# Performance work log

Hardware: AMD Instinct MI355X
Metric: run time of the kernel (lower is better)

Reference implementation:

```python
import jax, jax.numpy as jnp
import numpy as np

G = 32          # grid_size
H = 12          # num_heads
D = 768         # embed_dim
HD = D // H     # head_dim = 64
FF = 3072       # ff_dim
B, T = 2, 2048
SPAN = 2 * G - 1        # 63
SPAN_C = 4 * G + 1      # 129
EPS = 1e-5


def setup_inputs() -> dict:
    key = jax.random.key(0)
    ks = jax.random.split(key, 16)
    s = 0.02
    is_sep = jax.random.uniform(ks[6], (T,)) < 0.05
    demo_id = jax.random.randint(ks[5], (T,), 0, 8)
    demo_id = jnp.where(is_sep, -1, demo_id)
    return {
        'x': jax.random.normal(ks[0], (B, T, D), jnp.float32),
        'row': jax.random.randint(ks[1], (T,), 0, G),
        'col': jax.random.randint(ks[2], (T,), 0, G),
        'demo_row': jax.random.randint(ks[3], (T,), 0, G),
        'demo_col': jax.random.randint(ks[4], (T,), 0, 2 * G),
        'demo_id': demo_id,
        'is_sep': is_sep,
        'ln1_w': jnp.ones((D,), jnp.float32),
        'ln1_b': jnp.zeros((D,), jnp.float32),
        'ln2_w': jnp.ones((D,), jnp.float32),
        'ln2_b': jnp.zeros((D,), jnp.float32),
        'qkv_w': jax.random.normal(ks[7], (D, 3 * D), jnp.float32) * s,
        'qkv_b': jnp.zeros((3 * D,), jnp.float32),
        'proj_w': jax.random.normal(ks[8], (D, D), jnp.float32) * s,
        'proj_b': jnp.zeros((D,), jnp.float32),
        'ff1_w': jax.random.normal(ks[9], (D, FF), jnp.float32) * s,
        'ff1_b': jnp.zeros((FF,), jnp.float32),
        'ff2_w': jax.random.normal(ks[10], (FF, D), jnp.float32) * s,
        'ff2_b': jnp.zeros((D,), jnp.float32),
        'rel_emb': jax.random.normal(ks[11], (SPAN * SPAN, H), jnp.float32) * s,
        'demo_emb': jax.random.normal(ks[12], (SPAN_C * SPAN, H), jnp.float32) * s,
    }


def _ln(x, w, b):
    m = jnp.mean(x, -1, keepdims=True)
    v = jnp.mean((x - m) ** 2, -1, keepdims=True)
    return (x - m) / jnp.sqrt(v + EPS) * w + b


def _rel_bias(rel_emb, row, col, is_sep):
    g1 = G - 1
    dr = jnp.clip(row[:, None] - row[None, :], -g1, g1) + g1
    dc = jnp.clip(col[:, None] - col[None, :], -g1, g1) + g1
    bias = rel_emb[dr * SPAN + dc]              # (T, T, H)
    valid = ~is_sep
    vp = (valid[:, None] & valid[None, :]).astype(jnp.float32)
    return jnp.transpose(bias, (2, 0, 1)) * vp[None]  # (H, T, T)


def _demo_bias(demo_emb, drow, dcol, did, is_sep):
    g1 = G - 1
    dr = jnp.clip(drow[:, None] - drow[None, :], -g1, g1) + g1
    dc = jnp.clip(dcol[:, None] - dcol[None, :], -2 * G, 2 * G) + 2 * G
    bias = demo_emb[dr * SPAN_C + dc]           # (T, T, H)
    valid = ~is_sep
    same = (did[:, None] == did[None, :]) & (did[:, None] >= 0) & (did[None, :] >= 0)
    vp = (valid[:, None] & valid[None, :] & same).astype(jnp.float32)
    return jnp.transpose(bias, (2, 0, 1)) * vp[None]


def reference(x, row, col, demo_row, demo_col, demo_id, is_sep,
              ln1_w, ln1_b, ln2_w, ln2_b, qkv_w, qkv_b, proj_w, proj_b,
              ff1_w, ff1_b, ff2_w, ff2_b, rel_emb, demo_emb):
    b, t, d = x.shape
    h1 = _ln(x, ln1_w, ln1_b)
    qkv = h1 @ qkv_w + qkv_b                        # (B, T, 3D)
    q, k, v = jnp.split(qkv, 3, axis=-1)
    q = q.reshape(b, t, H, HD).transpose(0, 2, 1, 3)  # (B, H, T, HD)
    k = k.reshape(b, t, H, HD).transpose(0, 2, 1, 3)
    v = v.reshape(b, t, H, HD).transpose(0, 2, 1, 3)
    scale = float(HD) ** -0.5
    logits = jnp.einsum('bhqd,bhkd->bhqk', q, k) * scale
    bias = _rel_bias(rel_emb, row, col, is_sep) + _demo_bias(demo_emb, demo_row, demo_col, demo_id, is_sep)
    attn = jax.nn.softmax(logits + bias[None], axis=-1)
    out = jnp.einsum('bhqk,bhkd->bhqd', attn, v)
    out = out.transpose(0, 2, 1, 3).reshape(b, t, D)
    out = out @ proj_w + proj_b
    x = x + out
    h2 = _ln(x, ln2_w, ln2_b)
    ff = jax.nn.gelu(h2 @ ff1_w + ff1_b, approximate=False) @ ff2_w + ff2_b
    return x + ff
```

## Files before the change

kernel.cpp:

```cpp
#include <hip/hip_runtime.h>
#include <hip/hip_bf16.h>
#include <hip/hip_fp16.h>
#include <math.h>

#define G_ 32
#define H_ 12
#define D_ 768
#define HD_ 64
#define FF_ 3072
#define B_ 2
#define T_ 2048
#define SPAN_ 63
#define SPANC_ 129
#define EPSF 1e-5f

typedef short bf16x8 __attribute__((ext_vector_type(8)));
typedef short short4v __attribute__((ext_vector_type(4)));
typedef float f32x4 __attribute__((ext_vector_type(4)));

__device__ __forceinline__ short f2bf(float f) {
    unsigned u = __builtin_bit_cast(unsigned, f);
    u = u + 0x7FFFu + ((u >> 16) & 1u);
    return (short)(u >> 16);
}

__device__ __forceinline__ unsigned char f2e5m2(float f) {
    unsigned short u = __half_as_ushort(__float2half(f));
    u = (unsigned short)(u + 0x7F + ((u >> 8) & 1));
    return (unsigned char)(u >> 8);
}
__device__ __forceinline__ float e5m2f(unsigned u) {
    return __half2float(__ushort_as_half((unsigned short)(u << 8)));
}

__device__ __forceinline__ void gl_lds16(const void* g, void* l) {
    __builtin_amdgcn_global_load_lds(
        (const __attribute__((address_space(1))) unsigned int*)g,
        (__attribute__((address_space(3))) unsigned int*)l, 16, 0, 0);
}

__global__ __launch_bounds__(256) void ln_bf16_kernel(const float* __restrict__ x,
                                                      const float* __restrict__ w,
                                                      const float* __restrict__ b,
                                                      short* __restrict__ out) {
    int wv = threadIdx.x >> 6;
    int lane = threadIdx.x & 63;
    int rowi = blockIdx.x * 4 + wv;
    const float* xr = x + (size_t)rowi * D_;
    float vals[12];
    float s = 0.f;
#pragma unroll
    for (int i = 0; i < 12; ++i) { vals[i] = xr[lane + i * 64]; s += vals[i]; }
#pragma unroll
    for (int off = 32; off > 0; off >>= 1) s += __shfl_xor(s, off, 64);
    float mean = s * (1.0f / D_);
    float vs = 0.f;
#pragma unroll
    for (int i = 0; i < 12; ++i) { float d = vals[i] - mean; vs += d * d; }
#pragma unroll
    for (int off = 32; off > 0; off >>= 1) vs += __shfl_xor(vs, off, 64);
    float rstd = rsqrtf(vs * (1.0f / D_) + EPSF);
    short* outr = out + (size_t)rowi * D_;
#pragma unroll
    for (int i = 0; i < 12; ++i) {
        int c = lane + i * 64;
        outr[c] = f2bf((vals[i] - mean) * rstd * w[c] + b[c]);
    }
}

__global__ __launch_bounds__(256) void tcast_all(const float* __restrict__ qkv_w,
                                                 const float* __restrict__ proj_w,
                                                 const float* __restrict__ ff1_w,
                                                 const float* __restrict__ ff2_w,
                                                 short* __restrict__ qkvt,
                                                 short* __restrict__ projt,
                                                 short* __restrict__ ff1t,
                                                 short* __restrict__ ff2t) {
    __shared__ float t[32][33];
    int bid = blockIdx.x;
    const float* W;
    short* Wt;
    int K, N, bx, lo;
    if (bid < 1728)      { W = qkv_w;  Wt = qkvt;  K = D_;  N = 3 * D_; bx = 72; lo = 0; }
    else if (bid < 2304) { W = proj_w; Wt = projt; K = D_;  N = D_;     bx = 24; lo = 1728; }
    else if (bid < 4608) { W = ff1_w;  Wt = ff1t;  K = D_;  N = FF_;    bx = 96; lo = 2304; }
    else                 { W = ff2_w;  Wt = ff2t;  K = FF_; N = D_;     bx = 24; lo = 4608; }
    int rblk = bid - lo;
    int n0 = (rblk % bx) * 32, k0 = (rblk / bx) * 32;
    int tid = threadIdx.x;
    int r = tid >> 3, c4 = (tid & 7) * 4;
    float4 v = *(const float4*)(W + (size_t)(k0 + r) * N + n0 + c4);
    t[r][c4 + 0] = v.x; t[r][c4 + 1] = v.y; t[r][c4 + 2] = v.z; t[r][c4 + 3] = v.w;
    __syncthreads();
    short4v o;
    o[0] = f2bf(t[c4 + 0][r]); o[1] = f2bf(t[c4 + 1][r]);
    o[2] = f2bf(t[c4 + 2][r]); o[3] = f2bf(t[c4 + 3][r]);
    *(short4v*)(Wt + (size_t)(n0 + r) * K + k0 + c4) = o;
}

__global__ __launch_bounds__(256) void bias_build(
    const int* __restrict__ rowp, const int* __restrict__ colp,
    const int* __restrict__ drowp, const int* __restrict__ dcolp,
    const int* __restrict__ didp,
    const float* __restrict__ rel_emb, const float* __restrict__ demo_emb,
    unsigned char* __restrict__ biasT) {
    __shared__ unsigned char patch[12][16][80];
    int k0 = blockIdx.x * 64, q0 = blockIdx.y * 16;
    int tid = threadIdx.x;
    int qi = tid >> 4, kq = (tid & 15) * 4;
    int q = q0 + qi;
    int idq = didp[q];
    int rq = rowp[q], cq = colp[q], drq = drowp[q], dcq = dcolp[q];
    float bvs[4][12];
#pragma unroll
    for (int j = 0; j < 4; ++j) {
        int k = k0 + kq + j;
        int idk = didp[k];
        float4 v0 = {0.f, 0.f, 0.f, 0.f}, v1 = v0, v2 = v0;
        if (idq >= 0 && idk >= 0) {
            int dr = min(max(rq - rowp[k], -(G_ - 1)), G_ - 1) + (G_ - 1);
            int dc = min(max(cq - colp[k], -(G_ - 1)), G_ - 1) + (G_ - 1);
            const float* rp = rel_emb + (size_t)(dr * SPAN_ + dc) * 12;
            v0 = *(const float4*)rp;
            v1 = *(const float4*)(rp + 4);
            v2 = *(const float4*)(rp + 8);
            if (idq == idk) {
                int ddr = min(max(drq - drowp[k], -(G_ - 1)), G_ - 1) + (G_ - 1);
                int ddc = min(max(dcq - dcolp[k], -2 * G_), 2 * G_) + 2 * G_;
                const float* dp = demo_emb + (size_t)(ddr * SPANC_ + ddc) * 12;
                float4 w0 = *(const float4*)dp;
                float4 w1 = *(const float4*)(dp + 4);
                float4 w2 = *(const float4*)(dp + 8);
                v0.x += w0.x; v0.y += w0.y; v0.z += w0.z; v0.w += w0.w;
                v1.x += w1.x; v1.y += w1.y; v1.z += w1.z; v1.w += w1.w;
                v2.x += w2.x; v2.y += w2.y; v2.z += w2.z; v2.w += w2.w;
            }
        }
        bvs[j][0] = v0.x; bvs[j][1] = v0.y; bvs[j][2] = v0.z; bvs[j][3] = v0.w;
        bvs[j][4] = v1.x; bvs[j][5] = v1.y; bvs[j][6] = v1.z; bvs[j][7] = v1.w;
        bvs[j][8] = v2.x; bvs[j][9] = v2.y; bvs[j][10] = v2.z; bvs[j][11] = v2.w;
    }
#pragma unroll
    for (int h = 0; h < 12; ++h) {
        uchar4 pk;
        pk.x = f2e5m2(bvs[0][h]); pk.y = f2e5m2(bvs[1][h]);
        pk.z = f2e5m2(bvs[2][h]); pk.w = f2e5m2(bvs[3][h]);
        *(uchar4*)&patch[h][qi][kq] = pk;
    }
    __syncthreads();
    for (int c = tid; c < 768; c += 256) {
        int rowid = c >> 2, off = (c & 3) * 16;
        int h = rowid >> 4, q2 = rowid & 15;
        *(uint4*)(biasT + (size_t)h * T_ * T_ + (size_t)(q0 + q2) * T_ + k0 + off) =
            *(const uint4*)&patch[h][q2][off];
    }
}

enum { EPI_NONE = 0, EPI_RES = 1, EPI_GELU = 2 };

template <int EPI, int BF16OUT, int BM>
__global__ __launch_bounds__(256, 2) void gemm_bf16(const short* __restrict__ A,
                                                    const short* __restrict__ Bt,
                                                    const float* __restrict__ bias,
                                                    const float* __restrict__ res,
                                                    void* __restrict__ Cv,
                                                    int M, int N, int K) {
    __shared__ short As[BM * 64];
    __shared__ short Bs[128 * 64];
    constexpr int WM = BM / 2;
    constexpr int MF = WM / 16;
    int tid = threadIdx.x;
    int l = tid & 63;
    int w = tid >> 6;
    int wm = w >> 1, wn = w & 1;
    int row0 = blockIdx.y * BM, col0 = blockIdx.x * 128;
    int g = l >> 4, c16 = l & 15;
    f32x4 zero = {0.f, 0.f, 0.f, 0.f};
    f32x4 acc[MF][4];
#pragma unroll
    for (int m = 0; m < MF; ++m)
#pragma unroll
        for (int n = 0; n < 4; ++n) acc[m][n] = zero;

    int srowA = w * (BM / 4) + (l >> 3);
    int srowB = w * 32 + (l >> 3);
    int sseg0 = (l & 7);

    for (int k0 = 0; k0 < K; k0 += 64) {
#pragma unroll
        for (int inst = 0; inst < BM / 32; ++inst) {
            int arow = srowA + inst * 8;
            int seg = sseg0 ^ (arow & 7);
            gl_lds16(A + (size_t)(row0 + arow) * K + k0 + seg * 8,
                     &As[(w * (BM / 4) + inst * 8) * 64]);
        }
#pragma unroll
        for (int inst = 0; inst < 4; ++inst) {
            int brow = srowB + inst * 8;
            int seg = sseg0 ^ (brow & 7);
            gl_lds16(Bt + (size_t)(col0 + brow) * K + k0 + seg * 8,
                     &Bs[(w * 32 + inst * 8) * 64]);
        }
        __syncthreads();
#pragma unroll
        for (int dk = 0; dk < 2; ++dk) {
            bf16x8 af[MF], bfr[4];
#pragma unroll
            for (int m = 0; m < MF; ++m) {
                int r = wm * WM + m * 16 + c16;
                af[m] = *(const bf16x8*)&As[r * 64 + (((dk * 4 + g) ^ (r & 7)) << 3)];
            }
#pragma unroll
            for (int n = 0; n < 4; ++n) {
                int r = wn * 64 + n * 16 + c16;
                bfr[n] = *(const bf16x8*)&Bs[r * 64 + (((dk * 4 + g) ^ (r & 7)) << 3)];
            }
#pragma unroll
            for (int m = 0; m < MF; ++m)
#pragma unroll
                for (int n = 0; n < 4; ++n)
                    acc[m][n] = __builtin_amdgcn_mfma_f32_16x16x32_bf16(af[m], bfr[n], acc[m][n], 0, 0, 0);
        }
        __syncthreads();
    }

#pragma unroll
    for (int m = 0; m < MF; ++m)
#pragma unroll
        for (int n = 0; n < 4; ++n) {
            int rrow = row0 + wm * WM + m * 16 + g * 4;
            int ccol = col0 + wn * 64 + n * 16 + c16;
            float bv = bias[ccol];
#pragma unroll
            for (int i = 0; i < 4; ++i) {
                float v = acc[m][n][i] + bv;
                if (EPI == EPI_GELU) v = 0.5f * v * (1.f + erff(v * 0.70710678118f));
                if (EPI == EPI_RES) v += res[(size_t)(rrow + i) * N + ccol];
                if (BF16OUT)
                    ((short*)Cv)[(size_t)(rrow + i) * N + ccol] = f2bf(v);
                else
                    ((float*)Cv)[(size_t)(rrow + i) * N + ccol] = v;
            }
        }
}

__global__ __launch_bounds__(256, 3) void attn_mfma(
    const short* __restrict__ qkv,
    const unsigned char* __restrict__ biasT,
    short* __restrict__ attn_o) {
    __shared__ short Ks[2][64 * 64];
    __shared__ short Vt[2][64 * 72];
    __shared__ short Pb[4][16 * 72];

    int tid = threadIdx.x, w = tid >> 6, l = tid & 63;
    int g = l >> 4, c16 = l & 15;
    int bid = blockIdx.x;
    int nb = (bid & 7) * 96 + (bid >> 3);
    int qt = nb & 31, bh = nb >> 5;
    int h = bh % H_, b = bh / H_;
    int q0 = qt * 64;
    const int QS = 3 * D_;
    const short* kvbase = qkv + (size_t)b * T_ * QS;

    bf16x8 qf[2];
    {
        int qrow = q0 + w * 16 + c16;
        const short* qp = kvbase + (size_t)qrow * QS + h * HD_;
        qf[0] = *(const bf16x8*)(qp + g * 8);
        qf[1] = *(const bf16x8*)(qp + 32 + g * 8);
    }
    const unsigned char* bptr[4];
#pragma unroll
    for (int i = 0; i < 4; ++i)
        bptr[i] = biasT + (size_t)h * T_ * T_ + (size_t)(q0 + w * 16 + g * 4 + i) * T_;

    int krow = tid >> 3, kseg = tid & 7;
    int kx = (kseg ^ (krow & 7)) << 3;
    const short* kgp = kvbase + D_ + h * HD_ + kseg * 8;
    int vk0 = (tid & 31) * 2, vd0 = (tid >> 5) * 8;
    int vbase = ((((vk0 >> 3) ^ (vd0 >> 3)) & 7) << 3) + (vk0 & 7);
    const short* vgp = kvbase + 2 * D_ + h * HD_ + vd0;

    f32x4 zero = {0.f, 0.f, 0.f, 0.f};
    f32x4 oacc[4];
#pragma unroll
    for (int nf = 0; nf < 4; ++nf) oacc[nf] = zero;
    float lsum[4] = {0.f, 0.f, 0.f, 0.f};

    bf16x8 kr0, kr1, vr0, vr1;
    kr0 = *(const bf16x8*)(kgp + (size_t)krow * QS);
    kr1 = *(const bf16x8*)(kgp + (size_t)(krow + 32) * QS);
    vr0 = *(const bf16x8*)(vgp + (size_t)vk0 * QS);
    vr1 = *(const bf16x8*)(vgp + (size_t)(vk0 + 1) * QS);
    *(bf16x8*)&Ks[0][krow * 64 + kx] = kr0;
    *(bf16x8*)&Ks[0][(krow + 32) * 64 + kx] = kr1;
#pragma unroll
    for (int j = 0; j < 8; ++j) {
        unsigned pr = (unsigned)(ushort)vr0[j] | ((unsigned)(ushort)vr1[j] << 16);
        *(unsigned*)&Vt[0][(vd0 + j) * 72 + vbase] = pr;
    }
    {
        const short* kg1 = kgp + (size_t)64 * QS;
        const short* vg1 = vgp + (size_t)64 * QS;
        kr0 = *(const bf16x8*)(kg1 + (size_t)krow * QS);
        kr1 = *(const bf16x8*)(kg1 + (size_t)(krow + 32) * QS);
        vr0 = *(const bf16x8*)(vg1 + (size_t)vk0 * QS);
        vr1 = *(const bf16x8*)(vg1 + (size_t)(vk0 + 1) * QS);
    }

    for (int t = 0; t < 32; ++t) {
        __syncthreads();
        const short* KsC = Ks[t & 1];
        const short* VtC = Vt[t & 1];
        short* KsN = Ks[(t + 1) & 1];
        short* VtN = Vt[(t + 1) & 1];
        *(bf16x8*)&KsN[krow * 64 + kx] = kr0;
        *(bf16x8*)&KsN[(krow + 32) * 64 + kx] = kr1;
#pragma unroll
        for (int j = 0; j < 8; ++j) {
            unsigned pr = (unsigned)(ushort)vr0[j] | ((unsigned)(ushort)vr1[j] << 16);
            *(unsigned*)&VtN[(vd0 + j) * 72 + vbase] = pr;
        }
        {
            int kb2 = ((t + 2) & 31) * 64;
            const short* kg2 = kgp + (size_t)kb2 * QS;
            const short* vg2 = vgp + (size_t)kb2 * QS;
            kr0 = *(const bf16x8*)(kg2 + (size_t)krow * QS);
            kr1 = *(const bf16x8*)(kg2 + (size_t)(krow + 32) * QS);
            vr0 = *(const bf16x8*)(vg2 + (size_t)vk0 * QS);
            vr1 = *(const bf16x8*)(vg2 + (size_t)(vk0 + 1) * QS);
        }
        int kb = t * 64;
        float bv[16];
#pragma unroll
        for (int nf = 0; nf < 4; ++nf)
#pragma unroll
            for (int i = 0; i < 4; ++i)
                bv[nf * 4 + i] = e5m2f(bptr[i][kb + nf * 16 + c16]);
        f32x4 sac[4];
#pragma unroll
        for (int nf = 0; nf < 4; ++nf) sac[nf] = zero;
#pragma unroll
        for (int dk = 0; dk < 2; ++dk) {
#pragma unroll
            for (int nf = 0; nf < 4; ++nf) {
                int r = nf * 16 + c16;
                bf16x8 kf = *(const bf16x8*)&KsC[r * 64 + (((dk * 4 + g) ^ (r & 7)) << 3)];
                sac[nf] = __builtin_amdgcn_mfma_f32_16x16x32_bf16(qf[dk], kf, sac[nf], 0, 0, 0);
            }
        }
#pragma unroll
        for (int nf = 0; nf < 4; ++nf)
#pragma unroll
            for (int i = 0; i < 4; ++i) {
                float e = __expf(fmaf(sac[nf][i], 0.125f, bv[nf * 4 + i]));
                sac[nf][i] = e;
                lsum[i] += e;
            }
        short* pbw = &Pb[w][0];
#pragma unroll
        for (int nf = 0; nf < 4; ++nf) {
            int chunkbase = nf * 2 + (c16 >> 3);
            int kpos = c16 & 7;
#pragma unroll
            for (int i = 0; i < 4; ++i)
                pbw[(g * 4 + i) * 72 + (((chunkbase ^ g) & 7) << 3) + kpos] = f2bf(sac[nf][i]);
        }
#pragma unroll
        for (int dk = 0; dk < 2; ++dk) {
            bf16x8 pa = *(const bf16x8*)&pbw[c16 * 72 + (((dk * 4 + g) ^ (c16 >> 2)) & 7) * 8];
#pragma unroll
            for (int nf = 0; nf < 4; ++nf) {
                int d = nf * 16 + c16;
                bf16x8 vb = *(const bf16x8*)&VtC[d * 72 + (((dk * 4 + g) ^ (d >> 3)) & 7) * 8];
                oacc[nf] = __builtin_amdgcn_mfma_f32_16x16x32_bf16(pa, vb, oacc[nf], 0, 0, 0);
            }
        }
    }

#pragma unroll
    for (int i = 0; i < 4; ++i) {
#pragma unroll
        for (int off = 1; off < 16; off <<= 1) lsum[i] += __shfl_xor(lsum[i], off, 64);
    }

#pragma unroll
    for (int nf = 0; nf < 4; ++nf)
#pragma unroll
        for (int i = 0; i < 4; ++i) {
            float o = oacc[nf][i] / lsum[i];
            int qq = q0 + w * 16 + g * 4 + i;
            attn_o[(size_t)(b * T_ + qq) * D_ + h * HD_ + nf * 16 + c16] = f2bf(o);
        }
}

extern "C" void kernel_launch(void* const* d_in, const int* in_sizes, int n_in,
                              void* d_out, int out_size, void* d_ws, size_t ws_size,
                              hipStream_t stream) {
    const float* x = (const float*)d_in[0];
    const int* rowp = (const int*)d_in[1];
    const int* colp = (const int*)d_in[2];
    const int* drowp = (const int*)d_in[3];
    const int* dcolp = (const int*)d_in[4];
    const int* didp = (const int*)d_in[5];
    const float* ln1_w = (const float*)d_in[7];
    const float* ln1_b = (const float*)d_in[8];
    const float* ln2_w = (const float*)d_in[9];
    const float* ln2_b = (const float*)d_in[10];
    const float* qkv_w = (const float*)d_in[11];
    const float* qkv_b = (const float*)d_in[12];
    const float* proj_w = (const float*)d_in[13];
    const float* proj_b = (const float*)d_in[14];
    const float* ff1_w = (const float*)d_in[15];
    const float* ff1_b = (const float*)d_in[16];
    const float* ff2_w = (const float*)d_in[17];
    const float* ff2_b = (const float*)d_in[18];
    const float* rel_emb = (const float*)d_in[19];
    const float* demo_emb = (const float*)d_in[20];
    float* out = (float*)d_out;

    const int M = B_ * T_;
    char* p = (char*)d_ws;
    short* h1 = (short*)p;     p += (size_t)M * D_ * 2;
    short* qkvb = (short*)p;   p += (size_t)M * 3 * D_ * 2;
    short* attn_o = (short*)p; p += (size_t)M * D_ * 2;
    short* qkvt = (short*)p;   p += (size_t)(3 * D_) * D_ * 2;
    short* projt = (short*)p;  p += (size_t)D_ * D_ * 2;
    short* ff1t = (short*)p;   p += (size_t)FF_ * D_ * 2;
    short* ff2t = (short*)p;   p += (size_t)D_ * FF_ * 2;
    float* x2 = (float*)p;
    short* h2 = (short*)(p + (size_t)M * D_ * 4);
    short* ffact = (short*)(p + (size_t)M * D_ * 4 + (size_t)M * D_ * 2);
    unsigned char* biasT = (unsigned char*)p;

    bias_build<<<dim3(T_ / 64, T_ / 16), 256, 0, stream>>>(
        rowp, colp, drowp, dcolp, didp, rel_emb, demo_emb, biasT);
    tcast_all<<<dim3(6912), 256, 0, stream>>>(qkv_w, proj_w, ff1_w, ff2_w,
                                              qkvt, projt, ff1t, ff2t);

    ln_bf16_kernel<<<dim3(M / 4), 256, 0, stream>>>(x, ln1_w, ln1_b, h1);

    gemm_bf16<EPI_NONE, 1, 128><<<dim3(3 * D_ / 128, M / 128), 256, 0, stream>>>(
        h1, qkvt, qkv_b, nullptr, qkvb, M, 3 * D_, D_);

    attn_mfma<<<dim3(B_ * H_ * (T_ / 64)), 256, 0, stream>>>(qkvb, biasT, attn_o);

    gemm_bf16<EPI_RES, 0, 64><<<dim3(D_ / 128, M / 64), 256, 0, stream>>>(
        attn_o, projt, proj_b, x, x2, M, D_, D_);

    ln_bf16_kernel<<<dim3(M / 4), 256, 0, stream>>>(x2, ln2_w, ln2_b, h2);

    gemm_bf16<EPI_GELU, 1, 128><<<dim3(FF_ / 128, M / 128), 256, 0, stream>>>(
        h2, ff1t, ff1_b, nullptr, ffact, M, FF_, D_);

    gemm_bf16<EPI_RES, 0, 64><<<dim3(D_ / 128, M / 64), 256, 0, stream>>>(
        ffact, ff2t, ff2_b, x2, out, M, D_, FF_);
}
```

Baseline: 238.7 us.

## Pre-transpose V into global buffer and load V fragments directly in attention

Adds a separate kernel that writes V transposed per (batch, head) into a new workspace buffer. The attention kernel then loads V MFMA operands straight from global memory each tile, dropping the LDS V staging, the in-register transpose and the V double buffer. Launch bounds rise from 3 to 4 waves per SIMD to use the freed LDS. The costs are an extra kernel launch, an extra round trip of V through memory, and uncoalesced strided per-lane global loads inside the loop with less latency hiding.

```diff
diff --git a/kernel.cpp b/kernel.cpp
--- a/kernel.cpp
+++ b/kernel.cpp
@@ -98,6 +98,23 @@
     *(short4v*)(Wt + (size_t)(n0 + r) * K + k0 + c4) = o;
 }
 
+__global__ __launch_bounds__(256) void vtrans_kernel(const short* __restrict__ qkvb,
+                                                     short* __restrict__ vt) {
+    __shared__ short t[32][36];
+    int bh = blockIdx.y;
+    int h = bh % H_, b = bh / H_;
+    int kt = blockIdx.x & 63, dt = blockIdx.x >> 6;
+    int k0 = kt * 32, d0 = dt * 32;
+    int tid = threadIdx.x;
+    int r = tid >> 3, c4 = (tid & 7) * 4;
+    *(short4v*)&t[r][c4] = *(const short4v*)(
+        qkvb + (size_t)(b * T_ + k0 + r) * (3 * D_) + 2 * D_ + h * HD_ + d0 + c4);
+    __syncthreads();
+    short4v o;
+    o[0] = t[c4 + 0][r]; o[1] = t[c4 + 1][r]; o[2] = t[c4 + 2][r]; o[3] = t[c4 + 3][r];
+    *(short4v*)(vt + (size_t)((b * H_ + h) * HD_ + d0 + r) * T_ + k0 + c4) = o;
+}
+
 __global__ __launch_bounds__(256) void bias_build(
     const int* __restrict__ rowp, const int* __restrict__ colp,
     const int* __restrict__ drowp, const int* __restrict__ dcolp,
@@ -244,12 +261,12 @@
         }
 }
 
-__global__ __launch_bounds__(256, 3) void attn_mfma(
+__global__ __launch_bounds__(256, 4) void attn_mfma(
     const short* __restrict__ qkv,
+    const short* __restrict__ vt,
     const unsigned char* __restrict__ biasT,
     short* __restrict__ attn_o) {
     __shared__ short Ks[2][64 * 64];
-    __shared__ short Vt[2][64 * 72];
     __shared__ short Pb[4][16 * 72];
 
     int tid = threadIdx.x, w = tid >> 6, l = tid & 63;
@@ -274,12 +291,15 @@
     for (int i = 0; i < 4; ++i)
         bptr[i] = biasT + (size_t)h * T_ * T_ + (size_t)(q0 + w * 16 + g * 4 + i) * T_;
 
+    const short* vgbase = vt + (size_t)(b * H_ + h) * HD_ * T_;
+    const short* vrow[4];
+#pragma unroll
+    for (int nf = 0; nf < 4; ++nf)
+        vrow[nf] = vgbase + (size_t)(nf * 16 + c16) * T_ + g * 8;
+
     int krow = tid >> 3, kseg = tid & 7;
     int kx = (kseg ^ (krow & 7)) << 3;
     const short* kgp = kvbase + D_ + h * HD_ + kseg * 8;
-    int vk0 = (tid & 31) * 2, vd0 = (tid >> 5) * 8;
-    int vbase = ((((vk0 >> 3) ^ (vd0 >> 3)) & 7) << 3) + (vk0 & 7);
-    const short* vgp = kvbase + 2 * D_ + h * HD_ + vd0;
 
     f32x4 zero = {0.f, 0.f, 0.f, 0.f};
     f32x4 oacc[4];
@@ -287,50 +307,32 @@
     for (int nf = 0; nf < 4; ++nf) oacc[nf] = zero;
     float lsum[4] = {0.f, 0.f, 0.f, 0.f};
 
-    bf16x8 kr0, kr1, vr0, vr1;
+    bf16x8 kr0, kr1;
     kr0 = *(const bf16x8*)(kgp + (size_t)krow * QS);
     kr1 = *(const bf16x8*)(kgp + (size_t)(krow + 32) * QS);
-    vr0 = *(const bf16x8*)(vgp + (size_t)vk0 * QS);
-    vr1 = *(const bf16x8*)(vgp + (size_t)(vk0 + 1) * QS);
     *(bf16x8*)&Ks[0][krow * 64 + kx] = kr0;
     *(bf16x8*)&Ks[0][(krow + 32) * 64 + kx] = kr1;
-#pragma unroll
-    for (int j = 0; j < 8; ++j) {
-        unsigned pr = (unsigned)(ushort)vr0[j] | ((unsigned)(ushort)vr1[j] << 16);
-        *(unsigned*)&Vt[0][(vd0 + j) * 72 + vbase] = pr;
-    }
-    {
-        const short* kg1 = kgp + (size_t)64 * QS;
-        const short* vg1 = vgp + (size_t)64 * QS;
-        kr0 = *(const bf16x8*)(kg1 + (size_t)krow * QS);
-        kr1 = *(const bf16x8*)(kg1 + (size_t)(krow + 32) * QS);
-        vr0 = *(const bf16x8*)(vg1 + (size_t)vk0 * QS);
-        vr1 = *(const bf16x8*)(vg1 + (size_t)(vk0 + 1) * QS);
-    }
+    kr0 = *(const bf16x8*)(kgp + (size_t)(64 + krow) * QS);
+    kr1 = *(const bf16x8*)(kgp + (size_t)(64 + krow + 32) * QS);
 
     for (int t = 0; t < 32; ++t) {
         __syncthreads();
+        int kb = t * 64;
+        bf16x8 vb[2][4];
+#pragma unroll
+        for (int dk = 0; dk < 2; ++dk)
+#pragma unroll
+            for (int nf = 0; nf < 4; ++nf)
+                vb[dk][nf] = *(const bf16x8*)(vrow[nf] + kb + dk * 32);
         const short* KsC = Ks[t & 1];
-        const short* VtC = Vt[t & 1];
         short* KsN = Ks[(t + 1) & 1];
-        short* VtN = Vt[(t + 1) & 1];
         *(bf16x8*)&KsN[krow * 64 + kx] = kr0;
         *(bf16x8*)&KsN[(krow + 32) * 64 + kx] = kr1;
-#pragma unroll
-        for (int j = 0; j < 8; ++j) {
-            unsigned pr = (unsigned)(ushort)vr0[j] | ((unsigned)(ushort)vr1[j] << 16);
-            *(unsigned*)&VtN[(vd0 + j) * 72 + vbase] = pr;
-        }
         {
             int kb2 = ((t + 2) & 31) * 64;
-            const short* kg2 = kgp + (size_t)kb2 * QS;
-            const short* vg2 = vgp + (size_t)kb2 * QS;
-            kr0 = *(const bf16x8*)(kg2 + (size_t)krow * QS);
-            kr1 = *(const bf16x8*)(kg2 + (size_t)(krow + 32) * QS);
-            vr0 = *(const bf16x8*)(vg2 + (size_t)vk0 * QS);
-            vr1 = *(const bf16x8*)(vg2 + (size_t)(vk0 + 1) * QS);
-        }
-        int kb = t * 64;
+            kr0 = *(const bf16x8*)(kgp + (size_t)(kb2 + krow) * QS);
+            kr1 = *(const bf16x8*)(kgp + (size_t)(kb2 + krow + 32) * QS);
+        }
         float bv[16];
 #pragma unroll
         for (int nf = 0; nf < 4; ++nf)
@@ -370,11 +372,8 @@
         for (int dk = 0; dk < 2; ++dk) {
             bf16x8 pa = *(const bf16x8*)&pbw[c16 * 72 + (((dk * 4 + g) ^ (c16 >> 2)) & 7) * 8];
 #pragma unroll
-            for (int nf = 0; nf < 4; ++nf) {
-                int d = nf * 16 + c16;
-                bf16x8 vb = *(const bf16x8*)&VtC[d * 72 + (((dk * 4 + g) ^ (d >> 3)) & 7) * 8];
-                oacc[nf] = __builtin_amdgcn_mfma_f32_16x16x32_bf16(pa, vb, oacc[nf], 0, 0, 0);
-            }
+            for (int nf = 0; nf < 4; ++nf)
+                oacc[nf] = __builtin_amdgcn_mfma_f32_16x16x32_bf16(pa, vb[dk][nf], oacc[nf], 0, 0, 0);
         }
     }
 
@@ -428,6 +427,7 @@
     short* projt = (short*)p;  p += (size_t)D_ * D_ * 2;
     short* ff1t = (short*)p;   p += (size_t)FF_ * D_ * 2;
     short* ff2t = (short*)p;   p += (size_t)D_ * FF_ * 2;
+    short* vtb = (short*)p;    p += (size_t)B_ * H_ * HD_ * T_ * 2;
     float* x2 = (float*)p;
     short* h2 = (short*)(p + (size_t)M * D_ * 4);
     short* ffact = (short*)(p + (size_t)M * D_ * 4 + (size_t)M * D_ * 2);
@@ -443,7 +443,9 @@
     gemm_bf16<EPI_NONE, 1, 128><<<dim3(3 * D_ / 128, M / 128), 256, 0, stream>>>(
         h1, qkvt, qkv_b, nullptr, qkvb, M, 3 * D_, D_);
 
-    attn_mfma<<<dim3(B_ * H_ * (T_ / 64)), 256, 0, stream>>>(qkvb, biasT, attn_o);
+    vtrans_kernel<<<dim3(128, B_ * H_), 256, 0, stream>>>(qkvb, vtb);
+
+    attn_mfma<<<dim3(B_ * H_ * (T_ / 64)), 256, 0, stream>>>(qkvb, vtb, biasT, attn_o);
 
     gemm_bf16<EPI_RES, 0, 64><<<dim3(D_ / 128, M / 64), 256, 0, stream>>>(
         attn_o, projt, proj_b, x, x2, M, D_, D_);
```

After: 286.0 us. 19.8% more time.
